# Kernel tuning notes

Hardware: AMD Instinct MI355X
Metric: run time of the kernel (lower is better)

Reference implementation:

```python
import jax, jax.numpy as jnp
import numpy as np

D_MODEL = 1024
NUM_HEADS = 16
HEAD_DIM = D_MODEL // NUM_HEADS


def setup_inputs() -> dict:
    key = jax.random.key(0)
    ks = jax.random.split(key, 8)
    B, S = 4, 1024
    scale = 1.0 / np.sqrt(D_MODEL)
    return {
        "x": jax.random.normal(ks[0], (B, S, D_MODEL), jnp.float32),
        "tokens": jax.random.normal(ks[1], (B, 1, D_MODEL), jnp.float32),
        "Wq": jax.random.normal(ks[2], (D_MODEL, D_MODEL), jnp.float32) * scale,
        "bq": jnp.zeros((D_MODEL,), jnp.float32),
        "Wk": jax.random.normal(ks[3], (D_MODEL, D_MODEL), jnp.float32) * scale,
        "bk": jnp.zeros((D_MODEL,), jnp.float32),
        "Wv": jax.random.normal(ks[4], (D_MODEL, D_MODEL), jnp.float32) * scale,
        "bv": jnp.zeros((D_MODEL,), jnp.float32),
    }


def _split_heads(t):
    # [B, S, D] -> [B, H, S, hd]
    B, S, _ = t.shape
    return t.reshape(B, S, NUM_HEADS, HEAD_DIM).transpose(0, 2, 1, 3)


def reference(x, tokens, Wq, bq, Wk, bk, Wv, bv):
    # Projections (torch Linear: y = x @ W.T + b)
    Q = _split_heads(x @ Wq.T + bq)          # [B,H,S,hd]
    K = _split_heads(x @ Wk.T + bk)
    V = _split_heads(x @ Wv.T + bv)
    tQ = _split_heads(tokens @ Wq.T + bq)    # [B,H,1,hd] -> broadcast
    tK = _split_heads(tokens @ Wk.T + bk)
    cQ = Q + tQ
    cK = K + tK
    scores = jnp.einsum("bhqd,bhkd->bhqk", cQ, cK) / jnp.sqrt(jnp.float32(HEAD_DIM))
    attn = jax.nn.softmax(scores, axis=-1)
    out = jnp.einsum("bhqk,bhkd->bhqd", attn, V)  # [B,H,S,hd]
    B, H, S, hd = out.shape
    return out.transpose(0, 2, 1, 3).reshape(B, S, D_MODEL)
```

## Files before the change

kernel.cpp:

```cpp
#include <hip/hip_runtime.h>
#include <hip/hip_bf16.h>


typedef __bf16 bf16;
typedef __bf16 bf16x8 __attribute__((ext_vector_type(8)));
typedef float  f32x4  __attribute__((ext_vector_type(4)));

#define LOG2E 1.4426950408889634f

__device__ __forceinline__ void gll16(const void* g, void* l) {
  __builtin_amdgcn_global_load_lds(
      (const __attribute__((address_space(1))) unsigned int*)g,
      (__attribute__((address_space(3))) unsigned int*)l, 16, 0, 0);
}

__device__ __forceinline__ unsigned cvtpk(float a, float b) {
  unsigned r;
  asm("v_cvt_pk_bf16_f32 %0, %1, %2" : "=v"(r) : "v"(a), "v"(b));
  return r;
}

__global__ void prep_kernel(const float* __restrict__ x, const float* __restrict__ tok,
                            const float* __restrict__ wq, const float* __restrict__ wk,
                            const float* __restrict__ wv,
                            bf16* __restrict__ xb, bf16* __restrict__ xt,
                            bf16* __restrict__ wdst) {
  const int bid = blockIdx.x;
  if (bid < 2048) {
    const size_t e = ((size_t)bid * 256 + threadIdx.x) * 8;
    const int b = (int)(e >> 20);
    const int d = (int)(e & 1023);
    const float4 a0 = *(const float4*)(x + e);
    const float4 a1 = *(const float4*)(x + e + 4);
    const float4 t0 = *(const float4*)(tok + b * 1024 + d);
    const float4 t1 = *(const float4*)(tok + b * 1024 + d + 4);
    bf16x8 vb, vt;
    vb[0]=(bf16)a0.x; vb[1]=(bf16)a0.y; vb[2]=(bf16)a0.z; vb[3]=(bf16)a0.w;
    vb[4]=(bf16)a1.x; vb[5]=(bf16)a1.y; vb[6]=(bf16)a1.z; vb[7]=(bf16)a1.w;
    vt[0]=(bf16)(a0.x+t0.x); vt[1]=(bf16)(a0.y+t0.y); vt[2]=(bf16)(a0.z+t0.z); vt[3]=(bf16)(a0.w+t0.w);
    vt[4]=(bf16)(a1.x+t1.x); vt[5]=(bf16)(a1.y+t1.y); vt[6]=(bf16)(a1.z+t1.z); vt[7]=(bf16)(a1.w+t1.w);
    *(bf16x8*)(xb + e) = vb;
    *(bf16x8*)(xt + e) = vt;
  } else {
    const size_t e = ((size_t)(bid - 2048) * 256 + threadIdx.x) * 8;
    const float* src; size_t off;
    if (e < (size_t)(1u<<20))      { src = wq; off = e; }
    else if (e < (size_t)(2u<<20)) { src = wk; off = e - (1u<<20); }
    else                           { src = wv; off = e - (2u<<20); }
    const float4 a0 = *(const float4*)(src + off);
    const float4 a1 = *(const float4*)(src + off + 4);
    bf16x8 v;
    v[0]=(bf16)a0.x; v[1]=(bf16)a0.y; v[2]=(bf16)a0.z; v[3]=(bf16)a0.w;
    v[4]=(bf16)a1.x; v[5]=(bf16)a1.y; v[6]=(bf16)a1.z; v[7]=(bf16)a1.w;
    *(bf16x8*)(wdst + e) = v;
  }
}

__global__ __launch_bounds__(256, 3) void qkv_gemm_kernel(
    const bf16* __restrict__ xt, const bf16* __restrict__ xb,
    const bf16* __restrict__ wq, const bf16* __restrict__ wk, const bf16* __restrict__ wv,
    const float* __restrict__ bq, const float* __restrict__ bk, const float* __restrict__ bv,
    bf16* __restrict__ cq, bf16* __restrict__ ck, bf16* __restrict__ vt)
{
  __shared__ __align__(16) char LDSG[49152];
  char* As = LDSG;
  char* Bs = LDSG + 24576;
  const int t = threadIdx.x, w = t >> 6, l = t & 63, g = l >> 4, c = l & 15;
  const int wr = w >> 1, wc = w & 1;
  const int wgid = blockIdx.x;
  const int xcd = wgid & 7;
  const int p = wgid >> 3;
  const int z = p >> 5;
  const int q = p & 31;
  const bf16 *A, *B; const float* bias; bf16* outp;
  int tm, tn;
  if (z < 2) { tm = xcd * 4 + (q & 3); tn = q >> 2; }
  else       { tm = q >> 2; tn = xcd * 4 + (q & 3); }
  if (z == 0)      { A = xt; B = wq; bias = bq; outp = cq; }
  else if (z == 1) { A = xt; B = wk; bias = bk; outp = ck; }
  else             { A = wv; B = xb; bias = bv; outp = vt; }
  const int m0 = tm * 128, n0 = tn * 128;

  f32x4 acc[4][4] = {};

  const int u = (t & 7) ^ ((t >> 3) & 7);
  const size_t ssw = (size_t)(2 * (t >> 3) + (u >> 2)) * 2048 + (size_t)(u & 3) * 16;
  const char* aga = (const char*)A + (size_t)m0 * 2048 + ssw;
  const char* bga = (const char*)B + (size_t)n0 * 2048 + ssw;

#define GSTAGE(slot, kt)                                                 \
  {                                                                      \
    const size_t ko = (size_t)(kt) * 64;            \
    char* ad = As + (slot) * 8192 + t * 16;                              \
    char* bd = Bs + (slot) * 8192 + t * 16;                              \
    gll16(aga + ko,          ad);                                        \
    gll16(aga + ko + 131072, ad + 4096);               \
    gll16(bga + ko,          bd);                                        \
    gll16(bga + ko + 131072, bd + 4096);                                 \
  }

  GSTAGE(0, 0);
  GSTAGE(1, 1);
  int st = 2;
  int s  = 0;
  for (int kt = 0; kt < 32; ++kt) {
    if (kt < 31) { asm volatile("s_waitcnt vmcnt(4)" ::: "memory"); }
    else         { asm volatile("s_waitcnt vmcnt(0)" ::: "memory"); }
    __builtin_amdgcn_sched_barrier(0);
    __builtin_amdgcn_s_barrier();
    if (kt < 30) GSTAGE(st, kt + 2);

    const char* Ab = As + s * 8192;
    const char* Bb = Bs + s * 8192;
    bf16x8 af[4], bfr[4];
#pragma unroll
    for (int mf = 0; mf < 4; ++mf) {
      const int mrow = wr * 64 + mf * 16 + c;
      af[mf] = *(const bf16x8*)(Ab + (mrow >> 1) * 128 +
                                (((((mrow & 1) << 2) + g) ^ ((mrow >> 1) & 7)) << 4));
    }
#pragma unroll
    for (int nf = 0; nf < 4; ++nf) {
      const int nrow = wc * 64 + nf * 16 + c;
      bfr[nf] = *(const bf16x8*)(Bb + (nrow >> 1) * 128 +
                                 (((((nrow & 1) << 2) + g) ^ ((nrow >> 1) & 7)) << 4));
    }
    __builtin_amdgcn_s_setprio(1);
#pragma unroll
    for (int mf = 0; mf < 4; ++mf)
#pragma unroll
      for (int nf = 0; nf < 4; ++nf)
        acc[mf][nf] = __builtin_amdgcn_mfma_f32_16x16x32_bf16(af[mf], bfr[nf], acc[mf][nf], 0, 0, 0);
    __builtin_amdgcn_s_setprio(0);
    s  = (s  == 2) ? 0 : s + 1;
    st = (st == 2) ? 0 : st + 1;
  }
#undef GSTAGE

  if (z < 2) {
    const float sc = (z == 0) ? 0.125f * LOG2E : 1.0f;
#pragma unroll
    for (int mf = 0; mf < 4; ++mf)
#pragma unroll
      for (int nf = 0; nf < 4; ++nf) {
        const int n = n0 + wc * 64 + nf * 16 + c;
        const int h = n >> 6, d = n & 63;
        const float bsum = 2.0f * bias[n];
#pragma unroll
        for (int r = 0; r < 4; ++r) {
          const int m = m0 + wr * 64 + mf * 16 + g * 4 + r;
          const int b = m >> 10, s2 = m & 1023;
          outp[(((size_t)(b * 16 + h)) * 1024 + s2) * 64 + d] = (bf16)((acc[mf][nf][r] + bsum) * sc);
        }
      }
  } else {
#pragma unroll
    for (int mf = 0; mf < 4; ++mf)
#pragma unroll
      for (int nf = 0; nf < 4; ++nf) {
        const int n = n0 + wc * 64 + nf * 16 + c;
        const int b = n >> 10, s2 = n & 1023;
#pragma unroll
        for (int r = 0; r < 4; ++r) {
          const int m = m0 + wr * 64 + mf * 16 + g * 4 + r;
          const int h = m >> 6, d = m & 63;
          outp[(((size_t)(b * 16 + h)) * 64 + d) * 1024 + s2] = (bf16)(acc[mf][nf][r] + bias[m]);
        }
      }
  }
}

__global__ __launch_bounds__(512) void attn_kernel(
    const bf16* __restrict__ cq, const bf16* __restrict__ ck, const bf16* __restrict__ vt,
    float* __restrict__ out)
{
  __shared__ __align__(16) char LDS[49152];
  const int t = threadIdx.x, w = t >> 6, l = t & 63, g = l >> 4, c = l & 15;
  const int wgid = blockIdx.x;
  const int xcd = wgid & 7;
  const int p_ = wgid >> 3;
  const int bh = xcd * 8 + (p_ >> 3);
  const int qt = p_ & 7;
  const int b = bh >> 4, h = bh & 15;
  const bf16* cqb = cq + (size_t)bh * 65536;
  const bf16* ckb = ck + (size_t)bh * 65536;
  const bf16* vtb = vt + (size_t)bh * 65536;
  const int q0 = qt * 128 + w * 16;

  bf16x8 qf[2];
#pragma unroll
  for (int kf = 0; kf < 2; ++kf)
    qf[kf] = *(const bf16x8*)(cqb + (size_t)(q0 + c) * 64 + kf * 32 + g * 8);

  f32x4 o[4] = {};
  float lsum = 0.f;

  const int r_ = t >> 3;
  const int sch = (t & 7) ^ (r_ & 7);
  const int kap = ((r_ >> 4) & 1) * 32 + ((r_ >> 2) & 3) * 8 + ((r_ >> 5) & 1) * 4 + (r_ & 3);
  const size_t ksrc = (size_t)kap * 128 + (size_t)sch * 16;
  const size_t vsrc = (size_t)r_ * 2048 + (size_t)sch * 16;

#define STAGE(slot, idx)                                                 \
  {                                                                      \
    const char* kgb = (const char*)ckb + (size_t)(idx) * 8192;           \
    const char* vgb = (const char*)vtb + (size_t)(idx) * 128;            \
    gll16(kgb + ksrc, LDS + (slot) * 8192 + t * 16);                     \
    gll16(vgb + vsrc, LDS + 24576 + (slot) * 8192 + t * 16);             \
  }

  STAGE(0, 0);
  STAGE(1, 1);
  int st = 2;
  int s  = 0;
  for (int idx = 0; idx < 16; ++idx) {
    if (idx < 15) { asm volatile("s_waitcnt vmcnt(2)" ::: "memory"); }
    else          { asm volatile("s_waitcnt vmcnt(0)" ::: "memory"); }
    __builtin_amdgcn_sched_barrier(0);
    __builtin_amdgcn_s_barrier();
    if (idx < 14) STAGE(st, idx + 2);

    const char* Kb = LDS + s * 8192;
    const char* Vb = LDS + 24576 + s * 8192;

    f32x4 sv[4] = {};
    __builtin_amdgcn_s_setprio(1);
#pragma unroll
    for (int kf = 0; kf < 2; ++kf)
#pragma unroll
      for (int nf = 0; nf < 4; ++nf) {
        const int kr = nf * 16 + c;
        bf16x8 kb = *(const bf16x8*)(Kb + kr * 128 + (((kf * 4 + g) ^ (kr & 7)) << 4));
        sv[nf] = __builtin_amdgcn_mfma_f32_16x16x32_bf16(kb, qf[kf], sv[nf], 0, 0, 0);
      }
    __builtin_amdgcn_s_setprio(0);

    float p[4][4];
#pragma unroll
    for (int nf = 0; nf < 4; ++nf)
#pragma unroll
      for (int r = 0; r < 4; ++r)
        p[nf][r] = exp2f(sv[nf][r]);
    const float s0_ = (p[0][0] + p[0][1]) + (p[0][2] + p[0][3]);
    const float s1_ = (p[1][0] + p[1][1]) + (p[1][2] + p[1][3]);
    const float s2_ = (p[2][0] + p[2][1]) + (p[2][2] + p[2][3]);
    const float s3_ = (p[3][0] + p[3][1]) + (p[3][2] + p[3][3]);
    lsum += (s0_ + s1_) + (s2_ + s3_);

    union { unsigned u[4]; bf16x8 v; } pa0, pa1;
    pa0.u[0] = cvtpk(p[0][0], p[0][1]); pa0.u[1] = cvtpk(p[0][2], p[0][3]);
    pa0.u[2] = cvtpk(p[2][0], p[2][1]); pa0.u[3] = cvtpk(p[2][2], p[2][3]);
    pa1.u[0] = cvtpk(p[1][0], p[1][1]); pa1.u[1] = cvtpk(p[1][2], p[1][3]);
    pa1.u[2] = cvtpk(p[3][0], p[3][1]); pa1.u[3] = cvtpk(p[3][2], p[3][3]);

    __builtin_amdgcn_s_setprio(1);
#pragma unroll
    for (int kf = 0; kf < 2; ++kf) {
      const bf16x8 pav = kf ? pa1.v : pa0.v;
#pragma unroll
      for (int nd = 0; nd < 4; ++nd) {
        const int vr = nd * 16 + c;
        bf16x8 vb = *(const bf16x8*)(Vb + vr * 128 + (((kf * 4 + g) ^ (vr & 7)) << 4));
        o[nd] = __builtin_amdgcn_mfma_f32_16x16x32_bf16(vb, pav, o[nd], 0, 0, 0);
      }
    }
    __builtin_amdgcn_s_setprio(0);

    s  = (s  == 2) ? 0 : s + 1;
    st = (st == 2) ? 0 : st + 1;
  }
#undef STAGE

  __syncthreads();

  lsum += __shfl_xor(lsum, 16, 64);
  lsum += __shfl_xor(lsum, 32, 64);
  const float inv = 1.0f / lsum;
  {
    char* Ob = LDS;
    const int row = w * 16 + c;
#pragma unroll
    for (int nd = 0; nd < 4; ++nd) {
      f32x4 vo = o[nd] * inv;
      const int pch = (nd * 4 + g) ^ (row & 7);
      *(f32x4*)(Ob + row * 256 + (pch << 4)) = vo;
    }
  }
  __syncthreads();
  {
    const int rr = t >> 2;
    float* orow = out + ((size_t)(b * 1024 + qt * 128 + rr)) * 1024 + h * 64;
#pragma unroll
    for (int i = 0; i < 4; ++i) {
      const int ch = (t & 3) + i * 4;
      f32x4 v = *(const f32x4*)(LDS + rr * 256 + ((ch ^ (rr & 7)) << 4));
      *(f32x4*)(orow + ch * 4) = v;
    }
  }
}

extern "C" void kernel_launch(void* const* d_in, const int* in_sizes, int n_in,
                              void* d_out, int out_size, void* d_ws, size_t ws_size,
                              hipStream_t stream) {
  const float* x   = (const float*)d_in[0];
  const float* tok = (const float*)d_in[1];
  const float* Wq  = (const float*)d_in[2];
  const float* bq  = (const float*)d_in[3];
  const float* Wk  = (const float*)d_in[4];
  const float* bk  = (const float*)d_in[5];
  const float* Wv  = (const float*)d_in[6];
  const float* bv  = (const float*)d_in[7];
  float* out = (float*)d_out;
  char* ws = (char*)d_ws;
  bf16* xt  = (bf16*)(ws + (size_t)0);
  bf16* xb  = (bf16*)(ws + ((size_t)8  << 20));
  bf16* wqb = (bf16*)(ws + ((size_t)16 << 20));
  bf16* wkb = (bf16*)(ws + ((size_t)18 << 20));
  bf16* wvb = (bf16*)(ws + ((size_t)20 << 20));
  bf16* cqw = (bf16*)(ws + ((size_t)22 << 20));
  bf16* ckw = (bf16*)(ws + ((size_t)30 << 20));
  bf16* vtw = (bf16*)(ws + ((size_t)38 << 20));

  prep_kernel<<<dim3(3584), dim3(256), 0, stream>>>(x, tok, Wq, Wk, Wv, xb, xt, wqb);
  qkv_gemm_kernel<<<dim3(768), dim3(256), 0, stream>>>(
      xt, xb, wqb, wkb, wvb, bq, bk, bv, cqw, ckw, vtw);
  attn_kernel<<<dim3(512), dim3(512), 0, stream>>>(cqw, ckw, vtw, out);
}
```

Measured before the change: 74.94 us.

## Fuse Q and K projection tiles to share the activation operand

The QKV GEMM now has each Q/K workgroup compute both the Q and K output tiles for the same 128x128 region. It stages the shared xt A-tile once alongside both weight tiles, which cuts A-operand global and LDS traffic for those tiles. The grid drops from 768 to 512 blocks, and the V tiles keep the old single-GEMM path. In exchange it uses more LDS (72KB), doubles the accumulator registers, and lowers the occupancy target to 2. Q/K blocks now do twice the work of V blocks, so load balance across the grid may suffer.

Result: faster. 72.46 us (median of 2 runs) (-3.3%).

```diff
diff --git a/kernel.cpp b/kernel.cpp
--- a/kernel.cpp
+++ b/kernel.cpp
@@ -56,104 +56,153 @@
   }
 }
 
-__global__ __launch_bounds__(256, 3) void qkv_gemm_kernel(
+__global__ __launch_bounds__(256, 2) void qkv_gemm_kernel(
     const bf16* __restrict__ xt, const bf16* __restrict__ xb,
     const bf16* __restrict__ wq, const bf16* __restrict__ wk, const bf16* __restrict__ wv,
     const float* __restrict__ bq, const float* __restrict__ bk, const float* __restrict__ bv,
     bf16* __restrict__ cq, bf16* __restrict__ ck, bf16* __restrict__ vt)
 {
-  __shared__ __align__(16) char LDSG[49152];
-  char* As = LDSG;
-  char* Bs = LDSG + 24576;
+  __shared__ __align__(16) char LDSG[73728];
+  char* As  = LDSG;
+  char* B0s = LDSG + 24576;
+  char* B1s = LDSG + 49152;
   const int t = threadIdx.x, w = t >> 6, l = t & 63, g = l >> 4, c = l & 15;
   const int wr = w >> 1, wc = w & 1;
   const int wgid = blockIdx.x;
   const int xcd = wgid & 7;
   const int p = wgid >> 3;
-  const int z = p >> 5;
-  const int q = p & 31;
-  const bf16 *A, *B; const float* bias; bf16* outp;
-  int tm, tn;
-  if (z < 2) { tm = xcd * 4 + (q & 3); tn = q >> 2; }
-  else       { tm = q >> 2; tn = xcd * 4 + (q & 3); }
-  if (z == 0)      { A = xt; B = wq; bias = bq; outp = cq; }
-  else if (z == 1) { A = xt; B = wk; bias = bk; outp = ck; }
-  else             { A = wv; B = xb; bias = bv; outp = vt; }
-  const int m0 = tm * 128, n0 = tn * 128;
-
-  f32x4 acc[4][4] = {};
 
   const int u = (t & 7) ^ ((t >> 3) & 7);
   const size_t ssw = (size_t)(2 * (t >> 3) + (u >> 2)) * 2048 + (size_t)(u & 3) * 16;
-  const char* aga = (const char*)A + (size_t)m0 * 2048 + ssw;
-  const char* bga = (const char*)B + (size_t)n0 * 2048 + ssw;
-
-#define GSTAGE(slot, kt)                                                 \
-  {                                                                      \
-    const size_t ko = (size_t)(kt) * 64;            \
-    char* ad = As + (slot) * 8192 + t * 16;                              \
-    char* bd = Bs + (slot) * 8192 + t * 16;                              \
-    gll16(aga + ko,          ad);                                        \
-    gll16(aga + ko + 131072, ad + 4096);               \
-    gll16(bga + ko,          bd);                                        \
-    gll16(bga + ko + 131072, bd + 4096);                                 \
-  }
-
-  GSTAGE(0, 0);
-  GSTAGE(1, 1);
-  int st = 2;
-  int s  = 0;
-  for (int kt = 0; kt < 32; ++kt) {
-    if (kt < 31) { asm volatile("s_waitcnt vmcnt(4)" ::: "memory"); }
-    else         { asm volatile("s_waitcnt vmcnt(0)" ::: "memory"); }
-    __builtin_amdgcn_sched_barrier(0);
-    __builtin_amdgcn_s_barrier();
-    if (kt < 30) GSTAGE(st, kt + 2);
-
-    const char* Ab = As + s * 8192;
-    const char* Bb = Bs + s * 8192;
-    bf16x8 af[4], bfr[4];
-#pragma unroll
-    for (int mf = 0; mf < 4; ++mf) {
-      const int mrow = wr * 64 + mf * 16 + c;
-      af[mf] = *(const bf16x8*)(Ab + (mrow >> 1) * 128 +
-                                (((((mrow & 1) << 2) + g) ^ ((mrow >> 1) & 7)) << 4));
-    }
-#pragma unroll
-    for (int nf = 0; nf < 4; ++nf) {
-      const int nrow = wc * 64 + nf * 16 + c;
-      bfr[nf] = *(const bf16x8*)(Bb + (nrow >> 1) * 128 +
-                                 (((((nrow & 1) << 2) + g) ^ ((nrow >> 1) & 7)) << 4));
-    }
-    __builtin_amdgcn_s_setprio(1);
-#pragma unroll
-    for (int mf = 0; mf < 4; ++mf)
-#pragma unroll
-      for (int nf = 0; nf < 4; ++nf)
-        acc[mf][nf] = __builtin_amdgcn_mfma_f32_16x16x32_bf16(af[mf], bfr[nf], acc[mf][nf], 0, 0, 0);
-    __builtin_amdgcn_s_setprio(0);
-    s  = (s  == 2) ? 0 : s + 1;
-    st = (st == 2) ? 0 : st + 1;
-  }
-#undef GSTAGE
-
-  if (z < 2) {
-    const float sc = (z == 0) ? 0.125f * LOG2E : 1.0f;
+
+#define FRAG(base, rowexpr)                                              \
+  (*(const bf16x8*)((base) + ((rowexpr) >> 1) * 128 +                    \
+    ((((((rowexpr) & 1) << 2) + g) ^ (((rowexpr) >> 1) & 7)) << 4)))
+
+  if (p < 32) {
+    const int tm = xcd * 4 + (p & 3), tn = p >> 2;
+    const int m0 = tm * 128, n0 = tn * 128;
+    const char* aga = (const char*)xt + (size_t)m0 * 2048 + ssw;
+    const char* bqa = (const char*)wq + (size_t)n0 * 2048 + ssw;
+    const char* bka = (const char*)wk + (size_t)n0 * 2048 + ssw;
+
+    f32x4 accQ[4][4] = {}, accK[4][4] = {};
+
+#define GSTAGE2(slot, kt)                                                \
+    {                                                                    \
+      const size_t ko = (size_t)(kt) * 64;                               \
+      char* ad = As  + (slot) * 8192 + t * 16;                           \
+      char* qd = B0s + (slot) * 8192 + t * 16;                           \
+      char* kd = B1s + (slot) * 8192 + t * 16;                           \
+      gll16(aga + ko,          ad);                                      \
+      gll16(aga + ko + 131072, ad + 4096);             \
+      gll16(bqa + ko,          qd);                                      \
+      gll16(bqa + ko + 131072, qd + 4096);                               \
+      gll16(bka + ko,          kd);                                      \
+      gll16(bka + ko + 131072, kd + 4096);                               \
+    }
+
+    GSTAGE2(0, 0);
+    GSTAGE2(1, 1);
+    int st = 2, s = 0;
+    for (int kt = 0; kt < 32; ++kt) {
+      if (kt < 31) { asm volatile("s_waitcnt vmcnt(6)" ::: "memory"); }
+      else         { asm volatile("s_waitcnt vmcnt(0)" ::: "memory"); }
+      __builtin_amdgcn_sched_barrier(0);
+      __builtin_amdgcn_s_barrier();
+      if (kt < 30) GSTAGE2(st, kt + 2);
+
+      const char* Ab = As  + s * 8192;
+      const char* Qb = B0s + s * 8192;
+      const char* Kb = B1s + s * 8192;
+      bf16x8 af[4], bq4[4], bk4[4];
+#pragma unroll
+      for (int mf = 0; mf < 4; ++mf) af[mf]  = FRAG(Ab, wr * 64 + mf * 16 + c);
+#pragma unroll
+      for (int nf = 0; nf < 4; ++nf) bq4[nf] = FRAG(Qb, wc * 64 + nf * 16 + c);
+#pragma unroll
+      for (int nf = 0; nf < 4; ++nf) bk4[nf] = FRAG(Kb, wc * 64 + nf * 16 + c);
+      __builtin_amdgcn_s_setprio(1);
+#pragma unroll
+      for (int mf = 0; mf < 4; ++mf)
+#pragma unroll
+        for (int nf = 0; nf < 4; ++nf) {
+          accQ[mf][nf] = __builtin_amdgcn_mfma_f32_16x16x32_bf16(af[mf], bq4[nf], accQ[mf][nf], 0, 0, 0);
+          accK[mf][nf] = __builtin_amdgcn_mfma_f32_16x16x32_bf16(af[mf], bk4[nf], accK[mf][nf], 0, 0, 0);
+        }
+      __builtin_amdgcn_s_setprio(0);
+      s  = (s  == 2) ? 0 : s + 1;
+      st = (st == 2) ? 0 : st + 1;
+    }
+#undef GSTAGE2
+
+    const float scq = 0.125f * LOG2E;
 #pragma unroll
     for (int mf = 0; mf < 4; ++mf)
 #pragma unroll
       for (int nf = 0; nf < 4; ++nf) {
         const int n = n0 + wc * 64 + nf * 16 + c;
         const int h = n >> 6, d = n & 63;
-        const float bsum = 2.0f * bias[n];
+        const float bq2 = 2.0f * bq[n];
+        const float bk2 = 2.0f * bk[n];
 #pragma unroll
         for (int r = 0; r < 4; ++r) {
           const int m = m0 + wr * 64 + mf * 16 + g * 4 + r;
           const int b = m >> 10, s2 = m & 1023;
-          outp[(((size_t)(b * 16 + h)) * 1024 + s2) * 64 + d] = (bf16)((acc[mf][nf][r] + bsum) * sc);
+          const size_t o = (((size_t)(b * 16 + h)) * 1024 + s2) * 64 + d;
+          cq[o] = (bf16)((accQ[mf][nf][r] + bq2) * scq);
+          ck[o] = (bf16)(accK[mf][nf][r] + bk2);
         }
       }
   } else {
+    const int q = p - 32;
+    const int tm = q >> 2, tn = xcd * 4 + (q & 3);
+    const int m0 = tm * 128, n0 = tn * 128;
+    const char* aga = (const char*)wv + (size_t)m0 * 2048 + ssw;
+    const char* bga = (const char*)xb + (size_t)n0 * 2048 + ssw;
+
+    f32x4 acc[4][4] = {};
+
+#define GSTAGE(slot, kt)                                                 \
+    {                                                                    \
+      const size_t ko = (size_t)(kt) * 64;                               \
+      char* ad = As  + (slot) * 8192 + t * 16;                           \
+      char* bd = B0s + (slot) * 8192 + t * 16;                           \
+      gll16(aga + ko,          ad);                                      \
+      gll16(aga + ko + 131072, ad + 4096);                               \
+      gll16(bga + ko,          bd);                                      \
+      gll16(bga + ko + 131072, bd + 4096);                               \
+    }
+
+    GSTAGE(0, 0);
+    GSTAGE(1, 1);
+    int st = 2, s = 0;
+    for (int kt = 0; kt < 32; ++kt) {
+      if (kt < 31) { asm volatile("s_waitcnt vmcnt(4)" ::: "memory"); }
+      else         { asm volatile("s_waitcnt vmcnt(0)" ::: "memory"); }
+      __builtin_amdgcn_sched_barrier(0);
+      __builtin_amdgcn_s_barrier();
+      if (kt < 30) GSTAGE(st, kt + 2);
+
+      const char* Ab = As  + s * 8192;
+      const char* Bb = B0s + s * 8192;
+      bf16x8 af[4], bfr[4];
+#pragma unroll
+      for (int mf = 0; mf < 4; ++mf) af[mf]  = FRAG(Ab, wr * 64 + mf * 16 + c);
+#pragma unroll
+      for (int nf = 0; nf < 4; ++nf) bfr[nf] = FRAG(Bb, wc * 64 + nf * 16 + c);
+      __builtin_amdgcn_s_setprio(1);
+#pragma unroll
+      for (int mf = 0; mf < 4; ++mf)
+#pragma unroll
+        for (int nf = 0; nf < 4; ++nf)
+          acc[mf][nf] = __builtin_amdgcn_mfma_f32_16x16x32_bf16(af[mf], bfr[nf], acc[mf][nf], 0, 0, 0);
+      __builtin_amdgcn_s_setprio(0);
+      s  = (s  == 2) ? 0 : s + 1;
+      st = (st == 2) ? 0 : st + 1;
+    }
+#undef GSTAGE
+
 #pragma unroll
     for (int mf = 0; mf < 4; ++mf)
 #pragma unroll
@@ -164,10 +213,11 @@
         for (int r = 0; r < 4; ++r) {
           const int m = m0 + wr * 64 + mf * 16 + g * 4 + r;
           const int h = m >> 6, d = m & 63;
-          outp[(((size_t)(b * 16 + h)) * 64 + d) * 1024 + s2] = (bf16)(acc[mf][nf][r] + bias[m]);
+          vt[(((size_t)(b * 16 + h)) * 64 + d) * 1024 + s2] = (bf16)(acc[mf][nf][r] + bv[m]);
         }
       }
   }
+#undef FRAG
 }
 
 __global__ __launch_bounds__(512) void attn_kernel(
@@ -322,7 +372,7 @@
   bf16* vtw = (bf16*)(ws + ((size_t)38 << 20));
 
   prep_kernel<<<dim3(3584), dim3(256), 0, stream>>>(x, tok, Wq, Wk, Wv, xb, xt, wqb);
-  qkv_gemm_kernel<<<dim3(768), dim3(256), 0, stream>>>(
+  qkv_gemm_kernel<<<dim3(512), dim3(256), 0, stream>>>(
       xt, xb, wqb, wkb, wvb, bq, bk, bv, cqw, ckw, vtw);
   attn_kernel<<<dim3(512), dim3(512), 0, stream>>>(cqw, ckw, vtw, out);
 }
```
